# Optimization experiments

Measured on AMD Instinct MI355X. Metric: run time of the kernel, lower is better.

Reference implementation:

```python
import math
import jax, jax.numpy as jnp
import numpy as np

B = 16; ENC_S = 64; ENC_T = 96
SCALE = 64; POOL = 16; DM = 256; NH = 16
E_LAYERS = 3; D_LAYERS = 2; DFF = 1024
OUT_S = 64; OUT_T = 32
LN_EPS = 1e-5


def _pe(d_model, length):
    pos = np.arange(length, dtype=np.float32)[:, None]
    div = np.exp(np.arange(0, d_model, 2, dtype=np.float32) * (-math.log(10000.0) / d_model))
    pe = np.zeros((length, d_model), np.float32)
    pe[:, 0::2] = np.sin(pos * div)
    pe[:, 1::2] = np.cos(pos * div)
    return jnp.asarray(pe)


def _conv1d_circ(x, w, b):
    # x: (N, C, L), w: (O, C, 3); torch Conv1d(padding=1, padding_mode='circular')
    xp = jnp.pad(x, ((0, 0), (0, 0), (1, 1)), mode='wrap')
    y = jax.lax.conv_general_dilated(xp, w, (1,), 'VALID',
                                     dimension_numbers=('NCH', 'OIH', 'NCH'))
    return y + b[None, :, None]


def _layernorm(x, w, b):
    mu = jnp.mean(x, -1, keepdims=True)
    var = jnp.var(x, -1, keepdims=True)
    return (x - mu) * jax.lax.rsqrt(var + LN_EPS) * w + b


def _data_embedding(x, sproj_w, sproj_b, scproj_w, scproj_b, tok_w, tok_b):
    Bb = x.shape[0]
    h = _conv1d_circ(jnp.swapaxes(x, 1, 2), sproj_w, sproj_b)       # (B, enc_t, enc_t)
    h = _conv1d_circ(h, scproj_w, scproj_b)                          # (B, scale, enc_t)
    h = _conv1d_circ(jnp.swapaxes(h, 1, 2), scproj_w, scproj_b)     # (B, scale, scale)
    h = h.reshape(Bb * SCALE, 1, SCALE)
    tok = jnp.swapaxes(_conv1d_circ(h, tok_w, tok_b), 1, 2)          # (B*scale, scale, dm)
    emb = tok + _pe(DM, SCALE)[None]
    return emb.reshape(Bb, SCALE, SCALE, DM)


def _lin_attn(q, k, v, causal):
    # q,k,v: (Bp, L, H, E); k/v adaptively avg-pooled over L to POOL (L % POOL == 0)
    Bp, L, H, E = q.shape
    win = L // POOL
    kp = k.reshape(Bp, POOL, win, H, E).mean(axis=2)
    vp = v.reshape(Bp, POOL, win, H, E).mean(axis=2)
    scores = jnp.einsum('blhe,bshe->bhls', q, kp)      # (Bp, H, L, POOL)
    if causal:
        m = jnp.arange(POOL)[None, :] > jnp.arange(L)[:, None]
        scores = jnp.where(m[None, None], -jnp.inf, scores)
    A = jax.nn.softmax(scores / math.sqrt(E), axis=-1)
    return jnp.einsum('bhls,bshd->blhd', A, vp)


def _st_attn(x, kv, Wq, bq, Wo, bo, causal):
    Bb, T, S, dm = x.shape
    H = NH // 2
    proj = lambda z: z @ Wq.T + bq
    # faithful to source: query_projection used for q, k AND v; views are flat reshapes
    qt = proj(x.reshape(Bb * S, T, dm)).reshape(Bb * S, T, H, -1)
    qs = proj(x.reshape(Bb * T, S, dm)).reshape(Bb * T, S, H, -1)
    kt = proj(kv.reshape(Bb * S, T, dm)).reshape(Bb * S, T, H, -1)
    ks = proj(kv.reshape(Bb * T, S, dm)).reshape(Bb * T, S, H, -1)
    out_t = _lin_attn(qt, kt, kt, causal).reshape(Bb, S, T, -1)
    out_s = _lin_attn(qs, ks, ks, causal).reshape(Bb, S, T, -1)
    out = jnp.concatenate([out_t, out_s], axis=-1).reshape(Bb, S * T, 2 * dm)
    out = out @ Wo.T + bo
    return out.reshape(Bb, T, S, dm)


def _ffn(x, c1w, c1b, c2w, c2b):
    # conv1d kernel_size=1 over the T axis of (B*S, T, dm) == pointwise GEMM
    Bb, T, S, dm = x.shape
    y = x.reshape(Bb * S, T, dm)
    y = jax.nn.gelu(jnp.einsum('ntd,fd->ntf', y, c1w) + c1b, approximate=False)
    y = jnp.einsum('ntf,df->ntd', y, c2w) + c2b
    return y.reshape(Bb, T, S, dm)


def _forward(x_enc, x_dec,
             enc_sproj_w, enc_sproj_b, enc_scproj_w, enc_scproj_b, enc_tok_w, enc_tok_b,
             dec_sproj_w, dec_sproj_b, dec_scproj_w, dec_scproj_b, dec_tok_w, dec_tok_b,
             e_Wq, e_bq, e_Wo, e_bo, e_c1w, e_c1b, e_c2w, e_c2b,
             e_ln1w, e_ln1b, e_ln2w, e_ln2b, enc_norm_w, enc_norm_b,
             d_sWq, d_sbq, d_sWo, d_sbo, d_cWq, d_cbq, d_cWo, d_cbo,
             d_c1w, d_c1b, d_c2w, d_c2b,
             d_ln1w, d_ln1b, d_ln2w, d_ln2b, d_ln3w, d_ln3b,
             dec_norm_w, dec_norm_b, proj_w, proj_b):
    enc = _data_embedding(x_enc, enc_sproj_w, enc_sproj_b, enc_scproj_w, enc_scproj_b, enc_tok_w, enc_tok_b)
    for i in range(E_LAYERS):
        h = enc + _st_attn(enc, enc, e_Wq[i], e_bq[i], e_Wo[i], e_bo[i], False)
        h = _layernorm(h, e_ln1w[i], e_ln1b[i])
        enc = _layernorm(h + _ffn(h, e_c1w[i], e_c1b[i], e_c2w[i], e_c2b[i]), e_ln2w[i], e_ln2b[i])
    enc = _layernorm(enc, enc_norm_w, enc_norm_b)
    dec = _data_embedding(x_dec, dec_sproj_w, dec_sproj_b, dec_scproj_w, dec_scproj_b, dec_tok_w, dec_tok_b)
    for i in range(D_LAYERS):
        h = dec + _st_attn(dec, dec, d_sWq[i], d_sbq[i], d_sWo[i], d_sbo[i], True)
        h = _layernorm(h, d_ln1w[i], d_ln1b[i])
        h = h + _st_attn(h, enc, d_cWq[i], d_cbq[i], d_cWo[i], d_cbo[i], False)
        h = _layernorm(h, d_ln2w[i], d_ln2b[i])
        dec = _layernorm(h + _ffn(h, d_c1w[i], d_c1b[i], d_c2w[i], d_c2b[i]), d_ln3w[i], d_ln3b[i])
    dec = _layernorm(dec, dec_norm_w, dec_norm_b)
    dec = dec.mean(axis=2)                 # (B, scale, dm)
    out = dec @ proj_w.T + proj_b          # (B, scale, out_s)
    return out[:, -OUT_T:, :]


def setup_inputs() -> dict:
    keys = iter(jax.random.split(jax.random.key(0), 80))
    def nrm(shape, s=0.02):
        return jax.random.normal(next(keys), shape, jnp.float32) * s
    E, D = E_LAYERS, D_LAYERS
    inp = {
        'x_enc': nrm((B, ENC_T, ENC_S), 1.0),
        'x_dec': nrm((B, ENC_T, ENC_S), 1.0),
    }
    for p in ('enc', 'dec'):
        inp[p + '_sproj_w'] = nrm((ENC_T, ENC_S, 3)); inp[p + '_sproj_b'] = nrm((ENC_T,))
        inp[p + '_scproj_w'] = nrm((SCALE, ENC_T, 3)); inp[p + '_scproj_b'] = nrm((SCALE,))
        inp[p + '_tok_w'] = nrm((DM, 1, 3), 0.1); inp[p + '_tok_b'] = nrm((DM,))
    inp.update(
        e_Wq=nrm((E, DM, DM)), e_bq=nrm((E, DM)),
        e_Wo=nrm((E, DM, 2 * DM)), e_bo=nrm((E, DM)),
        e_c1w=nrm((E, DFF, DM)), e_c1b=nrm((E, DFF)),
        e_c2w=nrm((E, DM, DFF)), e_c2b=nrm((E, DM)),
        e_ln1w=jnp.ones((E, DM)), e_ln1b=jnp.zeros((E, DM)),
        e_ln2w=jnp.ones((E, DM)), e_ln2b=jnp.zeros((E, DM)),
        enc_norm_w=jnp.ones((DM,)), enc_norm_b=jnp.zeros((DM,)),
        d_sWq=nrm((D, DM, DM)), d_sbq=nrm((D, DM)),
        d_sWo=nrm((D, DM, 2 * DM)), d_sbo=nrm((D, DM)),
        d_cWq=nrm((D, DM, DM)), d_cbq=nrm((D, DM)),
        d_cWo=nrm((D, DM, 2 * DM)), d_cbo=nrm((D, DM)),
        d_c1w=nrm((D, DFF, DM)), d_c1b=nrm((D, DFF)),
        d_c2w=nrm((D, DM, DFF)), d_c2b=nrm((D, DM)),
        d_ln1w=jnp.ones((D, DM)), d_ln1b=jnp.zeros((D, DM)),
        d_ln2w=jnp.ones((D, DM)), d_ln2b=jnp.zeros((D, DM)),
        d_ln3w=jnp.ones((D, DM)), d_ln3b=jnp.zeros((D, DM)),
        dec_norm_w=jnp.ones((DM,)), dec_norm_b=jnp.zeros((DM,)),
        proj_w=nrm((OUT_S, DM)), proj_b=nrm((OUT_S,)),
    )
    return inp


def reference(x_enc, x_dec,
              enc_sproj_w, enc_sproj_b, enc_scproj_w, enc_scproj_b, enc_tok_w, enc_tok_b,
              dec_sproj_w, dec_sproj_b, dec_scproj_w, dec_scproj_b, dec_tok_w, dec_tok_b,
              e_Wq, e_bq, e_Wo, e_bo, e_c1w, e_c1b, e_c2w, e_c2b,
              e_ln1w, e_ln1b, e_ln2w, e_ln2b, enc_norm_w, enc_norm_b,
              d_sWq, d_sbq, d_sWo, d_sbo, d_cWq, d_cbq, d_cWo, d_cbo,
              d_c1w, d_c1b, d_c2w, d_c2b,
              d_ln1w, d_ln1b, d_ln2w, d_ln2b, d_ln3w, d_ln3b,
              dec_norm_w, dec_norm_b, proj_w, proj_b):
    return _forward(x_enc, x_dec,
                    enc_sproj_w, enc_sproj_b, enc_scproj_w, enc_scproj_b, enc_tok_w, enc_tok_b,
                    dec_sproj_w, dec_sproj_b, dec_scproj_w, dec_scproj_b, dec_tok_w, dec_tok_b,
                    e_Wq, e_bq, e_Wo, e_bo, e_c1w, e_c1b, e_c2w, e_c2b,
                    e_ln1w, e_ln1b, e_ln2w, e_ln2b, enc_norm_w, enc_norm_b,
                    d_sWq, d_sbq, d_sWo, d_sbo, d_cWq, d_cbq, d_cWo, d_cbo,
                    d_c1w, d_c1b, d_c2w, d_c2b,
                    d_ln1w, d_ln1b, d_ln2w, d_ln2b, d_ln3w, d_ln3b,
                    dec_norm_w, dec_norm_b, proj_w, proj_b)
```

## Files before the change

### kernel.cpp

```cpp
#include <hip/hip_runtime.h>


typedef unsigned short u16;
typedef short s16;
typedef __attribute__((ext_vector_type(8))) s16 bfrag;
typedef __attribute__((ext_vector_type(4))) float f32x4;

__device__ __forceinline__ float b2f(u16 u) {
  union { float f; unsigned int i; } v; v.i = ((unsigned int)u) << 16; return v.f;
}
__device__ __forceinline__ u16 f2b(float f) {
  union { float f; unsigned int i; } v; v.f = f;
  unsigned int x = v.i;
  return (u16)((x + 0x7FFFu + ((x >> 16) & 1u)) >> 16);
}
__device__ __forceinline__ float gelu_f(float v) {
  float u = 0.7978845608f * v * (1.0f + 0.044715f * v * v);
  float e = __expf(2.0f * u);
  return v * (1.0f - 1.0f / (e + 1.0f));
}

__device__ __forceinline__ void gload16(const void* g, void* l) {
  __builtin_amdgcn_global_load_lds(
      (const __attribute__((address_space(1))) unsigned int*)g,
      (__attribute__((address_space(3))) unsigned int*)l, 16, 0, 0);
}

__global__ void ws_signal(float* out, float v) { out[0] = v; }

__global__ void cvt_all(const float* s0, const float* s1, const float* s2,
                        const float* s3, const float* s4, const float* s5,
                        const float* s6,
                        u16* d0, u16* d1, u16* d2, u16* d3, u16* d4, u16* d5,
                        u16* d6,
                        int n0, int n1, int n2, int n3, int n4, int n5, int n6) {
  const float* S[7] = {s0, s1, s2, s3, s4, s5, s6};
  u16* D[7] = {d0, d1, d2, d3, d4, d5, d6};
  int N[7] = {n0, n1, n2, n3, n4, n5, n6};
  int j = blockIdx.y;
  int i = blockIdx.x * 256 + threadIdx.x;
  if (i < N[j]) D[j][i] = f2b(S[j][i]);
}

__global__ void weff_all(const float* s0, const float* s1, const float* s2,
                         const float* s3, const float* s4, const float* s5,
                         const float* s6,
                         u16* d0, u16* d1, u16* d2, u16* d3, u16* d4, u16* d5,
                         u16* d6) {
  const float* S[7] = {s0, s1, s2, s3, s4, s5, s6};
  u16* D[7] = {d0, d1, d2, d3, d4, d5, d6};
  int j = blockIdx.y;
  int n = blockIdx.x, k = threadIdx.x;
  D[j][n * 256 + k] = f2b(S[j][n * 512 + k] + S[j][n * 512 + 256 + k]);
}

__global__ void pe_kernel(float* __restrict__ pe) {
  int l = blockIdx.x, d = threadIdx.x;
  int i = d >> 1;
  float div = expf((float)(2 * i) * (-9.210340371976184f / 256.0f));
  float ang = (float)l * div;
  pe[l * 256 + d] = (d & 1) ? cosf(ang) : sinf(ang);
}

__global__ void conv_sproj(const float* xe, const float* xd,
                           const float* we, const float* be,
                           const float* wd, const float* bd,
                           float* h1e, float* h1d) {
  int o = blockIdx.x, bb = blockIdx.y, l = threadIdx.x;
  int b = (bb < 16) ? bb : bb - 16;
  const float* x = (bb < 16) ? xe : xd;
  const float* w = (bb < 16) ? we : wd;
  const float* bi = (bb < 16) ? be : bd;
  float* h1 = (bb < 16) ? h1e : h1d;
  const float* wo = w + o * 192;
  const float* xb = x + (size_t)b * 96 * 64;
  float acc = bi[o];
#pragma unroll
  for (int k = 0; k < 3; ++k) {
    int lp = l + k - 1; if (lp < 0) lp += 96; if (lp >= 96) lp -= 96;
    const float* xr = xb + lp * 64;
    for (int c = 0; c < 64; ++c) acc = fmaf(xr[c], wo[c * 3 + k], acc);
  }
  h1[((size_t)b * 96 + o) * 96 + l] = acc;
}

__global__ void conv_scproj_t(const float* h1e, const float* h1d,
                              const float* we, const float* be,
                              const float* wd, const float* bd,
                              float* h2e, float* h2d) {
  int o = blockIdx.x, bb = blockIdx.y, l = threadIdx.x;
  int b = (bb < 16) ? bb : bb - 16;
  const float* h1 = (bb < 16) ? h1e : h1d;
  const float* w = (bb < 16) ? we : wd;
  const float* bi = (bb < 16) ? be : bd;
  float* h2 = (bb < 16) ? h2e : h2d;
  const float* wo = w + o * 288;
  const float* hb = h1 + (size_t)b * 96 * 96;
  float acc = bi[o];
#pragma unroll
  for (int k = 0; k < 3; ++k) {
    int lp = l + k - 1; if (lp < 0) lp += 96; if (lp >= 96) lp -= 96;
    for (int c = 0; c < 96; ++c) acc = fmaf(hb[c * 96 + lp], wo[c * 3 + k], acc);
  }
  h2[((size_t)b * 64 + o) * 96 + l] = acc;
}

__global__ void conv_scproj_s(const float* h2e, const float* h2d,
                              const float* we, const float* be,
                              const float* wd, const float* bd,
                              float* h3e, float* h3d) {
  int o = blockIdx.x, bb = blockIdx.y, l = threadIdx.x;
  int b = (bb < 16) ? bb : bb - 16;
  const float* h2 = (bb < 16) ? h2e : h2d;
  const float* w = (bb < 16) ? we : wd;
  const float* bi = (bb < 16) ? be : bd;
  float* h3 = (bb < 16) ? h3e : h3d;
  const float* wo = w + o * 288;
  const float* hb = h2 + (size_t)b * 64 * 96;
  float acc = bi[o];
#pragma unroll
  for (int k = 0; k < 3; ++k) {
    int lp = l + k - 1; if (lp < 0) lp += 64; if (lp >= 64) lp -= 64;
    for (int c = 0; c < 96; ++c) acc = fmaf(hb[lp * 96 + c], wo[c * 3 + k], acc);
  }
  h3[((size_t)b * 64 + o) * 64 + l] = acc;
}

__global__ void tok_embed(const float* h3e, const float* h3d,
                          const float* we, const float* be,
                          const float* wd, const float* bd,
                          const float* __restrict__ pe,
                          u16* Ee, u16* Ed) {
  int gg = blockIdx.x, d = threadIdx.x;
  int g = (gg < 1024) ? gg : gg - 1024;
  const float* h3 = (gg < 1024) ? h3e : h3d;
  const float* w = (gg < 1024) ? we : wd;
  const float* bi = (gg < 1024) ? be : bd;
  u16* E = (gg < 1024) ? Ee : Ed;
  __shared__ float row[64];
  if (d < 64) row[d] = h3[(size_t)g * 64 + d];
  __syncthreads();
  float w0 = w[d * 3], w1 = w[d * 3 + 1], w2 = w[d * 3 + 2], bd_ = bi[d];
  for (int j = 0; j < 64; ++j) {
    int jm = (j + 63) & 63, jp = (j + 1) & 63;
    float v = bd_ + row[jm] * w0 + row[j] * w1 + row[jp] * w2 + pe[j * 256 + d];
    E[((size_t)g * 64 + j) * 256 + d] = f2b(v);
  }
}

template <int ACT, int NBX>
__global__ __launch_bounds__(256) void mfma_gemm(const u16* __restrict__ A,
                                                 const u16* __restrict__ W,
                                                 const float* __restrict__ bias,
                                                 u16* __restrict__ C, int N, int K,
                                                 int nby) {
  __shared__ s16 smem[16384];
  s16* A0 = smem;        s16* A1 = smem + 4096;
  s16* B0 = smem + 8192; s16* B1 = smem + 12288;
  constexpr int LB = (NBX == 8) ? 3 : 1;
  int f = blockIdx.x;
  int q = (NBX * nby) >> 3;
  int w = (f & 7) * q + (f >> 3);
  int bx = w & (NBX - 1), by = w >> LB;
  int t = threadIdx.x;
  int wave = t >> 6, lane = t & 63;
  int wr = wave >> 1, wc = wave & 1;
  int row0 = by * 128, col0 = bx * 128;
  int kc = (lane >> 4) & 3, rr = lane & 15;
  const u16* Ap0 = A + (size_t)(row0 + wave * 16 + rr) * K + kc * 8;
  const u16* Ap1 = A + (size_t)(row0 + (wave + 4) * 16 + rr) * K + kc * 8;
  const u16* Bp0 = W + (size_t)(col0 + wave * 16 + rr) * K + kc * 8;
  const u16* Bp1 = W + (size_t)(col0 + (wave + 4) * 16 + rr) * K + kc * 8;
  f32x4 acc[4][4];
#pragma unroll
  for (int m = 0; m < 4; ++m)
#pragma unroll
    for (int n = 0; n < 4; ++n) acc[m][n] = (f32x4){0.f, 0.f, 0.f, 0.f};

  auto STAGE = [&](s16* a, s16* b, int kidx) {
    int k0 = kidx * 32;
    gload16(Ap0 + k0, a + wave * 512);
    gload16(Ap1 + k0, a + (wave + 4) * 512);
    gload16(Bp0 + k0, b + wave * 512);
    gload16(Bp1 + k0, b + (wave + 4) * 512);
  };
  int nk = K >> 5;
  auto STEP = [&](const s16* a, const s16* b, s16* sa, s16* sb, int ks) {
    if (ks + 1 < nk) asm volatile("s_waitcnt vmcnt(4)" ::: "memory");
    else             asm volatile("s_waitcnt vmcnt(0)" ::: "memory");
    __builtin_amdgcn_sched_barrier(0);
    __builtin_amdgcn_s_barrier();
    __builtin_amdgcn_sched_barrier(0);
    bfrag af[4], bf[4];
#pragma unroll
    for (int m = 0; m < 4; ++m) af[m] = *(const bfrag*)(a + ((wr * 4 + m) * 64 + lane) * 8);
#pragma unroll
    for (int n = 0; n < 4; ++n) bf[n] = *(const bfrag*)(b + ((wc * 4 + n) * 64 + lane) * 8);
    asm volatile("s_waitcnt lgkmcnt(0)" ::: "memory");
    __builtin_amdgcn_sched_barrier(0);
    __builtin_amdgcn_s_barrier();
    __builtin_amdgcn_sched_barrier(0);
    if (ks + 2 < nk) STAGE(sa, sb, ks + 2);
#pragma unroll
    for (int m = 0; m < 4; ++m)
#pragma unroll
      for (int n = 0; n < 4; ++n)
        acc[m][n] = __builtin_amdgcn_mfma_f32_16x16x32_bf16(af[m], bf[n], acc[m][n], 0, 0, 0);
  };

  STAGE(A0, B0, 0);
  STAGE(A1, B1, 1);
  for (int ks = 0; ks < nk; ks += 2) {
    STEP(A0, B0, A0, B0, ks);
    STEP(A1, B1, A1, B1, ks + 1);
  }
  s16* Cs = smem;
  int g4 = (lane >> 4) << 2;
  int cl = lane & 15;
  float bc[4];
#pragma unroll
  for (int n = 0; n < 4; ++n) bc[n] = bias[col0 + wc * 64 + n * 16 + cl];
#pragma unroll
  for (int P = 0; P < 4; ++P) {
    __syncthreads();
    if (wr == (P >> 1)) {
#pragma unroll
      for (int mm = 0; mm < 2; ++mm) {
        int m = (P & 1) * 2 + mm;
#pragma unroll
        for (int n = 0; n < 4; ++n) {
#pragma unroll
          for (int r = 0; r < 4; ++r) {
            float v = acc[m][n][r] + bc[n];
            if (ACT == 1) v = gelu_f(v);
            Cs[(mm * 16 + g4 + r) * 136 + wc * 64 + n * 16 + cl] = (s16)f2b(v);
          }
        }
      }
    }
    __syncthreads();
#pragma unroll
    for (int it = 0; it < 2; ++it) {
      int idx = it * 256 + t;
      int lr = idx >> 4, slot = idx & 15;
      *(uint4*)(C + (size_t)(row0 + P * 32 + lr) * N + col0 + slot * 8) =
          *(const uint4*)(Cs + lr * 136 + slot * 8);
    }
  }
}

__global__ __launch_bounds__(512) void mfma_gemm_resln(const u16* __restrict__ X,
                                                       const u16* __restrict__ W,
                                                       const float* __restrict__ bias,
                                                       u16* __restrict__ R,
                                                       const float* __restrict__ lnw,
                                                       const float* __restrict__ lnb,
                                                       int K) {
  __shared__ s16 smem[24576];
  __shared__ float pls[32][4][2];
  s16* A0 = smem;        s16* A1 = smem + 4096;
  s16* B0 = smem + 8192; s16* B1 = smem + 16384;
  int t = threadIdx.x;
  int wave = t >> 6, lane = t & 63;
  int wr = wave >> 2, wc = wave & 3;
  int row0 = blockIdx.x * 128;
  int kc = (lane >> 4) & 3, rr = lane & 15;
  const u16* Xp = X + (size_t)(row0 + wave * 16 + rr) * K + kc * 8;
  const u16* Wp0 = W + (size_t)(wave * 16 + rr) * K + kc * 8;
  const u16* Wp1 = W + (size_t)((wave + 8) * 16 + rr) * K + kc * 8;
  f32x4 acc[4][4];
#pragma unroll
  for (int m = 0; m < 4; ++m)
#pragma unroll
    for (int n = 0; n < 4; ++n) acc[m][n] = (f32x4){0.f, 0.f, 0.f, 0.f};

  auto STAGE = [&](s16* a, s16* b, int kidx) {
    int k0 = kidx * 32;
    gload16(Xp + k0, a + wave * 512);
    gload16(Wp0 + k0, b + wave * 512);
    gload16(Wp1 + k0, b + (wave + 8) * 512);
  };
  int nk = K >> 5;
  auto STEP = [&](const s16* a, const s16* b, s16* sa, s16* sb, int ks) {
    if (ks + 1 < nk) asm volatile("s_waitcnt vmcnt(3)" ::: "memory");
    else             asm volatile("s_waitcnt vmcnt(0)" ::: "memory");
    __builtin_amdgcn_sched_barrier(0);
    __builtin_amdgcn_s_barrier();
    __builtin_amdgcn_sched_barrier(0);
    bfrag af[4], bf[4];
#pragma unroll
    for (int m = 0; m < 4; ++m) af[m] = *(const bfrag*)(a + ((wr * 4 + m) * 64 + lane) * 8);
#pragma unroll
    for (int n = 0; n < 4; ++n) bf[n] = *(const bfrag*)(b + ((wc * 4 + n) * 64 + lane) * 8);
    asm volatile("s_waitcnt lgkmcnt(0)" ::: "memory");
    __builtin_amdgcn_sched_barrier(0);
    __builtin_amdgcn_s_barrier();
    __builtin_amdgcn_sched_barrier(0);
    if (ks + 2 < nk) STAGE(sa, sb, ks + 2);
#pragma unroll
    for (int m = 0; m < 4; ++m)
#pragma unroll
      for (int n = 0; n < 4; ++n)
        acc[m][n] = __builtin_amdgcn_mfma_f32_16x16x32_bf16(af[m], bf[n], acc[m][n], 0, 0, 0);
  };

  STAGE(A0, B0, 0);
  STAGE(A1, B1, 1);
  for (int ks = 0; ks < nk; ks += 2) {
    STEP(A0, B0, A0, B0, ks);
    STEP(A1, B1, A1, B1, ks + 1);
  }
  s16* Rs = smem;
  int g4 = (lane >> 4) << 2;
  int cl = lane & 15;
  float lw[4], lb[4], bc[4];
#pragma unroll
  for (int n = 0; n < 4; ++n) {
    int col = wc * 64 + n * 16 + cl;
    bc[n] = bias[col]; lw[n] = lnw[col]; lb[n] = lnb[col];
  }
#pragma unroll
  for (int P = 0; P < 4; ++P) {
    bool own = (wr == (P >> 1));
    __syncthreads();
#pragma unroll
    for (int it = 0; it < 2; ++it) {
      int idx = it * 512 + t;
      int lr = idx >> 5, slot = idx & 31;
      *(uint4*)(Rs + lr * 264 + slot * 8) =
          *(const uint4*)(R + (size_t)(row0 + P * 32 + lr) * 256 + slot * 8);
    }
    __syncthreads();
    if (own) {
#pragma unroll
      for (int mm = 0; mm < 2; ++mm) {
        int m = (P & 1) * 2 + mm;
#pragma unroll
        for (int r = 0; r < 4; ++r) {
          int lr = mm * 16 + g4 + r;
          float s = 0.f, s2 = 0.f;
#pragma unroll
          for (int n = 0; n < 4; ++n) {
            float v = acc[m][n][r] + bc[n] +
                      b2f((u16)Rs[lr * 264 + wc * 64 + n * 16 + cl]);
            acc[m][n][r] = v;
            s += v; s2 = fmaf(v, v, s2);
          }
#pragma unroll
          for (int o = 1; o < 16; o <<= 1) { s += __shfl_xor(s, o); s2 += __shfl_xor(s2, o); }
          if (cl == 0) { pls[lr][wc][0] = s; pls[lr][wc][1] = s2; }
        }
      }
    }
    __syncthreads();
    if (own) {
#pragma unroll
      for (int mm = 0; mm < 2; ++mm) {
        int m = (P & 1) * 2 + mm;
#pragma unroll
        for (int r = 0; r < 4; ++r) {
          int lr = mm * 16 + g4 + r;
          float s = pls[lr][0][0] + pls[lr][1][0] + pls[lr][2][0] + pls[lr][3][0];
          float s2 = pls[lr][0][1] + pls[lr][1][1] + pls[lr][2][1] + pls[lr][3][1];
          float mu = s * (1.0f / 256.0f);
          float var = fmaxf(s2 * (1.0f / 256.0f) - mu * mu, 0.0f);
          float rs = rsqrtf(var + 1e-5f);
#pragma unroll
          for (int n = 0; n < 4; ++n) {
            Rs[lr * 264 + wc * 64 + n * 16 + cl] =
                (s16)f2b((acc[m][n][r] - mu) * rs * lw[n] + lb[n]);
          }
        }
      }
    }
    __syncthreads();
#pragma unroll
    for (int it = 0; it < 2; ++it) {
      int idx = it * 512 + t;
      int lr = idx >> 5, slot = idx & 31;
      *(uint4*)(R + (size_t)(row0 + P * 32 + lr) * 256 + slot * 8) =
          *(const uint4*)(Rs + lr * 264 + slot * 8);
    }
  }
}

template <int CROSS, int CAUSAL>
__global__ __launch_bounds__(256) void qk_attn(const u16* __restrict__ A,
                                               const u16* __restrict__ Wq,
                                               const float* __restrict__ bq,
                                               u16* __restrict__ O,
                                               const u16* __restrict__ KP) {
  __shared__ s16 smem[27136];
  s16* Qs = smem;
  s16* As = smem + 16896;
  s16* Bs = smem + 18944;
  float* kp = (float*)(smem + 16896);
  int p = blockIdx.x, t = threadIdx.x;
  int wave = t >> 6, lane = t & 63;
  int wr = wave >> 1, wc = wave & 1;
  int kc = (lane >> 4) & 3, rr = lane & 15;
  const u16* Ap = A + (size_t)(p * 64 + wave * 16 + rr) * 256 + kc * 8;
  const u16* Wp = Wq + (size_t)rr * 256 + kc * 8;
  f32x4 acc[2][8];
#pragma unroll
  for (int m = 0; m < 2; ++m)
#pragma unroll
    for (int n = 0; n < 8; ++n) acc[m][n] = (f32x4){0.f, 0.f, 0.f, 0.f};

#pragma unroll
  for (int ks = 0; ks < 8; ++ks) {
    int k0 = ks * 32;
    gload16(Ap + k0, As + wave * 512);
#pragma unroll
    for (int i = 0; i < 4; ++i) {
      int fb = wave + i * 4;
      gload16(Wp + (size_t)fb * 16 * 256 + k0, Bs + fb * 512);
    }
    __syncthreads();
    bfrag a[2], b[8];
#pragma unroll
    for (int m = 0; m < 2; ++m) a[m] = *(const bfrag*)(As + ((wr * 2 + m) * 64 + lane) * 8);
#pragma unroll
    for (int n = 0; n < 8; ++n) b[n] = *(const bfrag*)(Bs + ((wc * 8 + n) * 64 + lane) * 8);
#pragma unroll
    for (int m = 0; m < 2; ++m)
#pragma unroll
      for (int n = 0; n < 8; ++n)
        acc[m][n] = __builtin_amdgcn_mfma_f32_16x16x32_bf16(a[m], b[n], acc[m][n], 0, 0, 0);
    __syncthreads();
  }
  int g4 = (lane >> 4) << 2;
  int cl = lane & 15;
#pragma unroll
  for (int m = 0; m < 2; ++m) {
#pragma unroll
    for (int n = 0; n < 8; ++n) {
      int col = wc * 128 + n * 16 + cl;
      float bcol = bq[col];
#pragma unroll
      for (int r = 0; r < 4; ++r) {
        int row = wr * 32 + m * 16 + g4 + r;
        Qs[row * 264 + col] = (s16)f2b(acc[m][n][r] + bcol);
      }
    }
  }
  __syncthreads();
  if (CROSS) {
    for (int idx = t; idx < 4096; idx += 256) {
      int s = idx >> 8, d = idx & 255;
      kp[s * 260 + d] = b2f(KP[((size_t)p * 16 + s) * 256 + d]);
    }
  } else {
    for (int idx = t; idx < 4096; idx += 256) {
      int s = idx >> 8, d = idx & 255;
      const s16* b0 = Qs + (4 * s) * 264 + d;
      kp[s * 260 + d] = 0.25f * (b2f((u16)b0[0]) + b2f((u16)b0[264]) +
                                 b2f((u16)b0[528]) + b2f((u16)b0[792]));
    }
  }
  __syncthreads();
#pragma unroll
  for (int pi = 0; pi < 2; ++pi) {
    int pp = t + pi * 256;
    int h = pp >> 6, l = pp & 63;
    s16* q = Qs + l * 264 + h * 32;
    float qr[32];
#pragma unroll
    for (int e = 0; e < 32; e += 4) {
      ushort4 v = *(const ushort4*)&q[e];
      qr[e] = b2f(v.x); qr[e + 1] = b2f(v.y); qr[e + 2] = b2f(v.z); qr[e + 3] = b2f(v.w);
    }
    float sc[16], mx = -INFINITY;
#pragma unroll
    for (int s = 0; s < 16; ++s) {
      const float* kpp = kp + s * 260 + h * 32;
      float d = 0.f;
#pragma unroll
      for (int e = 0; e < 32; ++e) d = fmaf(qr[e], kpp[e], d);
      d *= 0.17677669529663687f;
      if (CAUSAL && s > l) d = -INFINITY;
      sc[s] = d; mx = fmaxf(mx, d);
    }
    float sum = 0.f;
#pragma unroll
    for (int s = 0; s < 16; ++s) { sc[s] = expf(sc[s] - mx); sum += sc[s]; }
    float inv = 1.0f / sum;
    float o[32] = {};
#pragma unroll
    for (int s = 0; s < 16; ++s) {
      float a = sc[s] * inv;
      const float* vp = kp + s * 260 + h * 32;
#pragma unroll
      for (int e = 0; e < 32; ++e) o[e] = fmaf(a, vp[e], o[e]);
    }
#pragma unroll
    for (int e = 0; e < 32; e += 4) {
      ushort4 v;
      v.x = f2b(o[e]); v.y = f2b(o[e + 1]); v.z = f2b(o[e + 2]); v.w = f2b(o[e + 3]);
      *(ushort4*)&q[e] = v;
    }
  }
  __syncthreads();
  u16* Og = O + (size_t)p * 16384;
#pragma unroll
  for (int i = 0; i < 8; ++i) {
    int idx = i * 256 + t;
    int row = idx >> 5, slot = idx & 31;
    *(uint4*)(Og + row * 256 + slot * 8) = *(const uint4*)(Qs + row * 264 + slot * 8);
  }
}

__global__ __launch_bounds__(256) void ln_bf(u16* __restrict__ X,
                                             const float* __restrict__ w,
                                             const float* __restrict__ b) {
  int lane = threadIdx.x & 63, wv = threadIdx.x >> 6;
  size_t row = (size_t)blockIdx.x * 4 + wv;
  size_t off = row * 256 + lane * 4;
  ushort4 xv = *(const ushort4*)(X + off);
  float v0 = b2f(xv.x), v1 = b2f(xv.y), v2 = b2f(xv.z), v3 = b2f(xv.w);
  float s = v0 + v1 + v2 + v3;
  float s2 = v0 * v0 + v1 * v1 + v2 * v2 + v3 * v3;
#pragma unroll
  for (int o = 32; o; o >>= 1) { s += __shfl_xor(s, o); s2 += __shfl_xor(s2, o); }
  float mu = s * (1.0f / 256.0f);
  float var = fmaxf(s2 * (1.0f / 256.0f) - mu * mu, 0.0f);
  float rs = rsqrtf(var + 1e-5f);
  float4 w4 = *(const float4*)(w + lane * 4);
  float4 b4 = *(const float4*)(b + lane * 4);
  ushort4 o4;
  o4.x = f2b((v0 - mu) * rs * w4.x + b4.x);
  o4.y = f2b((v1 - mu) * rs * w4.y + b4.y);
  o4.z = f2b((v2 - mu) * rs * w4.z + b4.z);
  o4.w = f2b((v3 - mu) * rs * w4.w + b4.w);
  *(ushort4*)(X + off) = o4;
}

__global__ void pool_bf(const u16* __restrict__ A, u16* __restrict__ P) {
  int r = blockIdx.x, d = threadIdx.x;
  int g = r >> 4, s = r & 15;
  const u16* src = A + ((size_t)g * 64 + 4 * (size_t)s) * 256 + d;
  float v = 0.25f * (b2f(src[0]) + b2f(src[256]) + b2f(src[512]) + b2f(src[768]));
  P[(size_t)r * 256 + d] = f2b(v);
}

__global__ __launch_bounds__(256) void mean_proj_bf(const u16* __restrict__ X,
                                                    const float* __restrict__ pw,
                                                    const float* __restrict__ pb,
                                                    float* __restrict__ out) {
  int bid = blockIdx.x;
  int b = bid >> 5, ii = bid & 31;
  int i = 32 + ii;
  __shared__ float md[256];
  int d = threadIdx.x;
  const u16* base = X + ((size_t)b * 64 + i) * 64 * 256 + d;
  float s = 0.f;
  for (int j = 0; j < 64; ++j) s += b2f(base[(size_t)j * 256]);
  md[d] = s * (1.0f / 64.0f);
  __syncthreads();
  if (d < 64) {
    float acc = pb[d];
    const float* wr = pw + d * 256;
    for (int k = 0; k < 256; ++k) acc = fmaf(md[k], wr[k], acc);
    out[((size_t)b * 32 + ii) * 64 + d] = acc;
  }
}

extern "C" void kernel_launch(void* const* d_in, const int* in_sizes, int n_in,
                              void* d_out, int out_size, void* d_ws, size_t ws_size,
                              hipStream_t stream) {
  (void)in_sizes; (void)out_size;
  if (n_in < 50) return;

  const float* x_enc = (const float*)d_in[0];
  const float* x_dec = (const float*)d_in[1];
  const float* enc_sproj_w = (const float*)d_in[2];
  const float* enc_sproj_b = (const float*)d_in[3];
  const float* enc_scproj_w = (const float*)d_in[4];
  const float* enc_scproj_b = (const float*)d_in[5];
  const float* enc_tok_w = (const float*)d_in[6];
  const float* enc_tok_b = (const float*)d_in[7];
  const float* dec_sproj_w = (const float*)d_in[8];
  const float* dec_sproj_b = (const float*)d_in[9];
  const float* dec_scproj_w = (const float*)d_in[10];
  const float* dec_scproj_b = (const float*)d_in[11];
  const float* dec_tok_w = (const float*)d_in[12];
  const float* dec_tok_b = (const float*)d_in[13];
  const float* e_Wq = (const float*)d_in[14];
  const float* e_bq = (const float*)d_in[15];
  const float* e_Wo = (const float*)d_in[16];
  const float* e_bo = (const float*)d_in[17];
  const float* e_c1w = (const float*)d_in[18];
  const float* e_c1b = (const float*)d_in[19];
  const float* e_c2w = (const float*)d_in[20];
  const float* e_c2b = (const float*)d_in[21];
  const float* e_ln1w = (const float*)d_in[22];
  const float* e_ln1b = (const float*)d_in[23];
  const float* e_ln2w = (const float*)d_in[24];
  const float* e_ln2b = (const float*)d_in[25];
  const float* enc_norm_w = (const float*)d_in[26];
  const float* enc_norm_b = (const float*)d_in[27];
  const float* d_sWq = (const float*)d_in[28];
  const float* d_sbq = (const float*)d_in[29];
  const float* d_sWo = (const float*)d_in[30];
  const float* d_sbo = (const float*)d_in[31];
  const float* d_cWq = (const float*)d_in[32];
  const float* d_cbq = (const float*)d_in[33];
  const float* d_cWo = (const float*)d_in[34];
  const float* d_cbo = (const float*)d_in[35];
  const float* d_c1w = (const float*)d_in[36];
  const float* d_c1b = (const float*)d_in[37];
  const float* d_c2w = (const float*)d_in[38];
  const float* d_c2b = (const float*)d_in[39];
  const float* d_ln1w = (const float*)d_in[40];
  const float* d_ln1b = (const float*)d_in[41];
  const float* d_ln2w = (const float*)d_in[42];
  const float* d_ln2b = (const float*)d_in[43];
  const float* d_ln3w = (const float*)d_in[44];
  const float* d_ln3b = (const float*)d_in[45];
  const float* dec_norm_w = (const float*)d_in[46];
  const float* dec_norm_b = (const float*)d_in[47];
  const float* proj_w = (const float*)d_in[48];
  const float* proj_b = (const float*)d_in[49];

  const size_t ACT = 16777216;
  const size_t POOLE = 4194304;
  const size_t WBN = 3538944;
  size_t base_need = (3 * ACT + 2 * POOLE + WBN) * 2 +
                     (size_t)(16384 + 2 * (147456 + 98304 + 65536)) * 4;
  if (ws_size < base_need) {
    ws_signal<<<1, 1, 0, stream>>>((float*)d_out, (float)(ws_size >> 20));
    return;
  }
  char* wsb = (char*)d_ws;
  u16* A_enc = (u16*)wsb;  wsb += ACT * 2;
  u16* A_dec = (u16*)wsb;  wsb += ACT * 2;
  u16* T1 = (u16*)wsb;     wsb += ACT * 2;
  u16* PA = (u16*)wsb;     wsb += POOLE * 2;
  u16* PK = (u16*)wsb;     wsb += POOLE * 2;
  u16* WB = (u16*)wsb;     wsb += WBN * 2;
  float* PE = (float*)wsb;  wsb += 16384 * 4;
  float* EH1 = (float*)wsb; wsb += 147456 * 4;
  float* EH2 = (float*)wsb; wsb += 98304 * 4;
  float* EH3 = (float*)wsb; wsb += 65536 * 4;
  float* FH1 = (float*)wsb; wsb += 147456 * 4;
  float* FH2 = (float*)wsb; wsb += 98304 * 4;
  float* FH3 = (float*)wsb; wsb += 65536 * 4;

  int hf_rows = 16384;
  u16* HF = T1;
  if (ws_size >= base_need + (size_t)65536 * 1024 * 2) {
    hf_rows = 65536; HF = (u16*)wsb;
  } else if (ws_size >= base_need + (size_t)32768 * 1024 * 2) {
    hf_rows = 32768; HF = (u16*)wsb;
  }

  u16* eWq = WB;
  u16* eWeff = WB + 196608;
  u16* eC1 = WB + 393216;
  u16* eC2 = WB + 1179648;
  u16* dB = WB + 1966080;
  u16* dsWq = dB;
  u16* dsWeff = dB + 131072;
  u16* dcWq = dB + 262144;
  u16* dcWeff = dB + 393216;
  u16* dC1 = dB + 524288;
  u16* dC2 = dB + 1048576;

  cvt_all<<<dim3(3072, 7), 256, 0, stream>>>(
      e_Wq, e_c1w, e_c2w, d_sWq, d_cWq, d_c1w, d_c2w,
      eWq, eC1, eC2, dsWq, dcWq, dC1, dC2,
      196608, 786432, 786432, 131072, 131072, 524288, 524288);
  weff_all<<<dim3(256, 7), 256, 0, stream>>>(
      e_Wo, e_Wo + 131072, e_Wo + 262144, d_sWo, d_sWo + 131072,
      d_cWo, d_cWo + 131072,
      eWeff, eWeff + 65536, eWeff + 131072, dsWeff, dsWeff + 65536,
      dcWeff, dcWeff + 65536);

  pe_kernel<<<64, 256, 0, stream>>>(PE);

  conv_sproj<<<dim3(96, 32), 96, 0, stream>>>(x_enc, x_dec, enc_sproj_w, enc_sproj_b,
                                              dec_sproj_w, dec_sproj_b, EH1, FH1);
  conv_scproj_t<<<dim3(64, 32), 96, 0, stream>>>(EH1, FH1, enc_scproj_w, enc_scproj_b,
                                                 dec_scproj_w, dec_scproj_b, EH2, FH2);
  conv_scproj_s<<<dim3(64, 32), 64, 0, stream>>>(EH2, FH2, enc_scproj_w, enc_scproj_b,
                                                 dec_scproj_w, dec_scproj_b, EH3, FH3);
  tok_embed<<<2048, 256, 0, stream>>>(EH3, FH3, enc_tok_w, enc_tok_b,
                                      dec_tok_w, dec_tok_b, PE, A_enc, A_dec);

  for (int i = 0; i < 3; ++i) {
    qk_attn<0, 0><<<1024, 256, 0, stream>>>(A_enc, eWq + (size_t)i * 65536,
                                            e_bq + i * 256, T1, nullptr);
    mfma_gemm_resln<<<512, 512, 0, stream>>>(T1, eWeff + (size_t)i * 65536, e_bo + i * 256,
                                             A_enc, e_ln1w + i * 256, e_ln1b + i * 256, 256);
    for (int m0 = 0; m0 < 65536; m0 += hf_rows) {
      u16* Xc = A_enc + (size_t)m0 * 256;
      int nby = hf_rows / 128;
      mfma_gemm<1, 8><<<8 * nby, 256, 0, stream>>>(
          Xc, eC1 + (size_t)i * 262144, e_c1b + i * 1024, HF, 1024, 256, nby);
      mfma_gemm_resln<<<nby, 512, 0, stream>>>(
          HF, eC2 + (size_t)i * 262144, e_c2b + i * 256, Xc,
          e_ln2w + i * 256, e_ln2b + i * 256, 1024);
    }
  }
  ln_bf<<<16384, 256, 0, stream>>>(A_enc, enc_norm_w, enc_norm_b);
  pool_bf<<<16384, 256, 0, stream>>>(A_enc, PA);

  for (int i = 0; i < 2; ++i) {
    qk_attn<0, 1><<<1024, 256, 0, stream>>>(A_dec, dsWq + (size_t)i * 65536,
                                            d_sbq + i * 256, T1, nullptr);
    mfma_gemm_resln<<<512, 512, 0, stream>>>(T1, dsWeff + (size_t)i * 65536, d_sbo + i * 256,
                                             A_dec, d_ln1w + i * 256, d_ln1b + i * 256, 256);
    mfma_gemm<0, 2><<<256, 256, 0, stream>>>(PA, dcWq + (size_t)i * 65536,
                                             d_cbq + i * 256, PK, 256, 256, 128);
    qk_attn<1, 0><<<1024, 256, 0, stream>>>(A_dec, dcWq + (size_t)i * 65536,
                                            d_cbq + i * 256, T1, PK);
    mfma_gemm_resln<<<512, 512, 0, stream>>>(T1, dcWeff + (size_t)i * 65536, d_cbo + i * 256,
                                             A_dec, d_ln2w + i * 256, d_ln2b + i * 256, 256);
    for (int m0 = 0; m0 < 65536; m0 += hf_rows) {
      u16* Xc = A_dec + (size_t)m0 * 256;
      int nby = hf_rows / 128;
      mfma_gemm<1, 8><<<8 * nby, 256, 0, stream>>>(
          Xc, dC1 + (size_t)i * 262144, d_c1b + i * 1024, HF, 1024, 256, nby);
      mfma_gemm_resln<<<nby, 512, 0, stream>>>(
          HF, dC2 + (size_t)i * 262144, d_c2b + i * 256, Xc,
          d_ln3w + i * 256, d_ln3b + i * 256, 1024);
    }
  }
  ln_bf<<<16384, 256, 0, stream>>>(A_dec, dec_norm_w, dec_norm_b);

  mean_proj_bf<<<512, 256, 0, stream>>>(A_dec, proj_w, proj_b, (float*)d_out);
}
```

Before: 1.872 ms.

## Split Q projection from linear attention and use 256x256 tiles for FFN up-projection

The fused qk_attn kernel, which recomputed the Q projection with a small 64-row MFMA tile per block, is replaced by a separate mfma_gemm launch for the projection followed by a lighter lin_attn kernel that works in place on the projected tensor with 512 threads. The FFN first GEMM switches to a new 256x256-tile, 512-thread, double-buffered kernel with explicit waitcnt/barrier pipelining and a remapped block order. The goal is better MFMA utilisation and operand reuse in the GEMMs. The cost is an extra global round-trip of the Q tensor between kernels, plus extra launches.

```diff
diff --git a/kernel.cpp b/kernel.cpp
--- a/kernel.cpp
+++ b/kernel.cpp
@@ -249,6 +249,106 @@
   }
 }
 
+template <int ACT>
+__global__ __launch_bounds__(512) void mfma_gemm256(const u16* __restrict__ A,
+                                                    const u16* __restrict__ W,
+                                                    const float* __restrict__ bias,
+                                                    u16* __restrict__ C, int N, int K,
+                                                    int nby) {
+  __shared__ s16 smem[32768];
+  s16* A0 = smem;         s16* A1 = smem + 8192;
+  s16* B0 = smem + 16384; s16* B1 = smem + 24576;
+  int f = blockIdx.x;
+  int q = (4 * nby) >> 3;
+  int w = (f & 7) * q + (f >> 3);
+  int bx = w & 3, by = w >> 2;
+  int t = threadIdx.x;
+  int wave = t >> 6, lane = t & 63;
+  int wr = wave >> 2, wc = wave & 3;
+  int row0 = by * 256, col0 = bx * 256;
+  int kc = (lane >> 4) & 3, rr = lane & 15;
+  const u16* Ap0 = A + (size_t)(row0 + wave * 16 + rr) * K + kc * 8;
+  const u16* Ap1 = A + (size_t)(row0 + (wave + 8) * 16 + rr) * K + kc * 8;
+  const u16* Bp0 = W + (size_t)(col0 + wave * 16 + rr) * K + kc * 8;
+  const u16* Bp1 = W + (size_t)(col0 + (wave + 8) * 16 + rr) * K + kc * 8;
+  f32x4 acc[8][4];
+#pragma unroll
+  for (int m = 0; m < 8; ++m)
+#pragma unroll
+    for (int n = 0; n < 4; ++n) acc[m][n] = (f32x4){0.f, 0.f, 0.f, 0.f};
+
+  auto STAGE = [&](s16* a, s16* b, int kidx) {
+    int k0 = kidx * 32;
+    gload16(Ap0 + k0, a + wave * 512);
+    gload16(Ap1 + k0, a + (wave + 8) * 512);
+    gload16(Bp0 + k0, b + wave * 512);
+    gload16(Bp1 + k0, b + (wave + 8) * 512);
+  };
+  int nk = K >> 5;
+  auto STEP = [&](const s16* a, const s16* b, s16* sa, s16* sb, int ks) {
+    if (ks + 1 < nk) asm volatile("s_waitcnt vmcnt(4)" ::: "memory");
+    else             asm volatile("s_waitcnt vmcnt(0)" ::: "memory");
+    __builtin_amdgcn_sched_barrier(0);
+    __builtin_amdgcn_s_barrier();
+    __builtin_amdgcn_sched_barrier(0);
+    bfrag af[8], bf[4];
+#pragma unroll
+    for (int m = 0; m < 8; ++m) af[m] = *(const bfrag*)(a + ((wr * 8 + m) * 64 + lane) * 8);
+#pragma unroll
+    for (int n = 0; n < 4; ++n) bf[n] = *(const bfrag*)(b + ((wc * 4 + n) * 64 + lane) * 8);
+    asm volatile("s_waitcnt lgkmcnt(0)" ::: "memory");
+    __builtin_amdgcn_sched_barrier(0);
+    __builtin_amdgcn_s_barrier();
+    __builtin_amdgcn_sched_barrier(0);
+    if (ks + 2 < nk) STAGE(sa, sb, ks + 2);
+#pragma unroll
+    for (int m = 0; m < 8; ++m)
+#pragma unroll
+      for (int n = 0; n < 4; ++n)
+        acc[m][n] = __builtin_amdgcn_mfma_f32_16x16x32_bf16(af[m], bf[n], acc[m][n], 0, 0, 0);
+  };
+
+  STAGE(A0, B0, 0);
+  STAGE(A1, B1, 1);
+  for (int ks = 0; ks < nk; ks += 2) {
+    STEP(A0, B0, A0, B0, ks);
+    STEP(A1, B1, A1, B1, ks + 1);
+  }
+  s16* Cs = smem;
+  int g4 = (lane >> 4) << 2;
+  int cl = lane & 15;
+  float bc[4];
+#pragma unroll
+  for (int n = 0; n < 4; ++n) bc[n] = bias[col0 + wc * 64 + n * 16 + cl];
+#pragma unroll
+  for (int P = 0; P < 8; ++P) {
+    __syncthreads();
+    if (wr == (P >> 2)) {
+#pragma unroll
+      for (int mm = 0; mm < 2; ++mm) {
+        int m = (P & 3) * 2 + mm;
+#pragma unroll
+        for (int n = 0; n < 4; ++n) {
+#pragma unroll
+          for (int r = 0; r < 4; ++r) {
+            float v = acc[m][n][r] + bc[n];
+            if (ACT == 1) v = gelu_f(v);
+            Cs[(mm * 16 + g4 + r) * 264 + wc * 64 + n * 16 + cl] = (s16)f2b(v);
+          }
+        }
+      }
+    }
+    __syncthreads();
+#pragma unroll
+    for (int it = 0; it < 2; ++it) {
+      int idx = it * 512 + t;
+      int lr = idx >> 5, slot = idx & 31;
+      *(uint4*)(C + (size_t)(row0 + P * 32 + lr) * N + col0 + slot * 8) =
+          *(const uint4*)(Cs + lr * 264 + slot * 8);
+    }
+  }
+}
+
 __global__ __launch_bounds__(512) void mfma_gemm_resln(const u16* __restrict__ X,
                                                        const u16* __restrict__ W,
                                                        const float* __restrict__ bias,
@@ -385,128 +485,75 @@
 }
 
 template <int CROSS, int CAUSAL>
-__global__ __launch_bounds__(256) void qk_attn(const u16* __restrict__ A,
-                                               const u16* __restrict__ Wq,
-                                               const float* __restrict__ bq,
-                                               u16* __restrict__ O,
-                                               const u16* __restrict__ KP) {
-  __shared__ s16 smem[27136];
-  s16* Qs = smem;
-  s16* As = smem + 16896;
-  s16* Bs = smem + 18944;
-  float* kp = (float*)(smem + 16896);
+__global__ __launch_bounds__(512) void lin_attn(u16* __restrict__ Q,
+                                                const u16* __restrict__ KP) {
+  __shared__ u16 qs[64 * 264];
+  __shared__ float kpool[16][260];
   int p = blockIdx.x, t = threadIdx.x;
-  int wave = t >> 6, lane = t & 63;
-  int wr = wave >> 1, wc = wave & 1;
-  int kc = (lane >> 4) & 3, rr = lane & 15;
-  const u16* Ap = A + (size_t)(p * 64 + wave * 16 + rr) * 256 + kc * 8;
-  const u16* Wp = Wq + (size_t)rr * 256 + kc * 8;
-  f32x4 acc[2][8];
-#pragma unroll
-  for (int m = 0; m < 2; ++m)
-#pragma unroll
-    for (int n = 0; n < 8; ++n) acc[m][n] = (f32x4){0.f, 0.f, 0.f, 0.f};
-
-#pragma unroll
-  for (int ks = 0; ks < 8; ++ks) {
-    int k0 = ks * 32;
-    gload16(Ap + k0, As + wave * 512);
-#pragma unroll
-    for (int i = 0; i < 4; ++i) {
-      int fb = wave + i * 4;
-      gload16(Wp + (size_t)fb * 16 * 256 + k0, Bs + fb * 512);
-    }
-    __syncthreads();
-    bfrag a[2], b[8];
-#pragma unroll
-    for (int m = 0; m < 2; ++m) a[m] = *(const bfrag*)(As + ((wr * 2 + m) * 64 + lane) * 8);
-#pragma unroll
-    for (int n = 0; n < 8; ++n) b[n] = *(const bfrag*)(Bs + ((wc * 8 + n) * 64 + lane) * 8);
-#pragma unroll
-    for (int m = 0; m < 2; ++m)
-#pragma unroll
-      for (int n = 0; n < 8; ++n)
-        acc[m][n] = __builtin_amdgcn_mfma_f32_16x16x32_bf16(a[m], b[n], acc[m][n], 0, 0, 0);
-    __syncthreads();
-  }
-  int g4 = (lane >> 4) << 2;
-  int cl = lane & 15;
-#pragma unroll
-  for (int m = 0; m < 2; ++m) {
-#pragma unroll
-    for (int n = 0; n < 8; ++n) {
-      int col = wc * 128 + n * 16 + cl;
-      float bcol = bq[col];
-#pragma unroll
-      for (int r = 0; r < 4; ++r) {
-        int row = wr * 32 + m * 16 + g4 + r;
-        Qs[row * 264 + col] = (s16)f2b(acc[m][n][r] + bcol);
-      }
-    }
+  u16* Qg = Q + (size_t)p * 16384;
+#pragma unroll
+  for (int i = 0; i < 4; ++i) {
+    int idx = i * 512 + t;
+    int row = idx >> 5, slot = idx & 31;
+    *(uint4*)(qs + row * 264 + slot * 8) = *(const uint4*)(Qg + row * 256 + slot * 8);
   }
   __syncthreads();
   if (CROSS) {
-    for (int idx = t; idx < 4096; idx += 256) {
+    for (int idx = t; idx < 4096; idx += 512) {
       int s = idx >> 8, d = idx & 255;
-      kp[s * 260 + d] = b2f(KP[((size_t)p * 16 + s) * 256 + d]);
+      kpool[s][d] = b2f(KP[((size_t)p * 16 + s) * 256 + d]);
     }
   } else {
-    for (int idx = t; idx < 4096; idx += 256) {
+    for (int idx = t; idx < 4096; idx += 512) {
       int s = idx >> 8, d = idx & 255;
-      const s16* b0 = Qs + (4 * s) * 264 + d;
-      kp[s * 260 + d] = 0.25f * (b2f((u16)b0[0]) + b2f((u16)b0[264]) +
-                                 b2f((u16)b0[528]) + b2f((u16)b0[792]));
+      const u16* b0 = qs + (4 * s) * 264 + d;
+      kpool[s][d] = 0.25f * (b2f(b0[0]) + b2f(b0[264]) + b2f(b0[528]) + b2f(b0[792]));
     }
   }
   __syncthreads();
-#pragma unroll
-  for (int pi = 0; pi < 2; ++pi) {
-    int pp = t + pi * 256;
-    int h = pp >> 6, l = pp & 63;
-    s16* q = Qs + l * 264 + h * 32;
-    float qr[32];
-#pragma unroll
-    for (int e = 0; e < 32; e += 4) {
-      ushort4 v = *(const ushort4*)&q[e];
-      qr[e] = b2f(v.x); qr[e + 1] = b2f(v.y); qr[e + 2] = b2f(v.z); qr[e + 3] = b2f(v.w);
-    }
-    float sc[16], mx = -INFINITY;
-#pragma unroll
-    for (int s = 0; s < 16; ++s) {
-      const float* kpp = kp + s * 260 + h * 32;
-      float d = 0.f;
-#pragma unroll
-      for (int e = 0; e < 32; ++e) d = fmaf(qr[e], kpp[e], d);
-      d *= 0.17677669529663687f;
-      if (CAUSAL && s > l) d = -INFINITY;
-      sc[s] = d; mx = fmaxf(mx, d);
-    }
-    float sum = 0.f;
-#pragma unroll
-    for (int s = 0; s < 16; ++s) { sc[s] = expf(sc[s] - mx); sum += sc[s]; }
-    float inv = 1.0f / sum;
-    float o[32] = {};
-#pragma unroll
-    for (int s = 0; s < 16; ++s) {
-      float a = sc[s] * inv;
-      const float* vp = kp + s * 260 + h * 32;
-#pragma unroll
-      for (int e = 0; e < 32; ++e) o[e] = fmaf(a, vp[e], o[e]);
-    }
-#pragma unroll
-    for (int e = 0; e < 32; e += 4) {
-      ushort4 v;
-      v.x = f2b(o[e]); v.y = f2b(o[e + 1]); v.z = f2b(o[e + 2]); v.w = f2b(o[e + 3]);
-      *(ushort4*)&q[e] = v;
-    }
+  int h = t >> 6, l = t & 63;
+  u16* q = qs + l * 264 + h * 32;
+  float qr[32];
+#pragma unroll
+  for (int e = 0; e < 32; e += 4) {
+    ushort4 v = *(const ushort4*)&q[e];
+    qr[e] = b2f(v.x); qr[e + 1] = b2f(v.y); qr[e + 2] = b2f(v.z); qr[e + 3] = b2f(v.w);
+  }
+  float sc[16], mx = -INFINITY;
+#pragma unroll
+  for (int s = 0; s < 16; ++s) {
+    const float* kp = &kpool[s][h * 32];
+    float d = 0.f;
+#pragma unroll
+    for (int e = 0; e < 32; ++e) d = fmaf(qr[e], kp[e], d);
+    d *= 0.17677669529663687f;
+    if (CAUSAL && s > l) d = -INFINITY;
+    sc[s] = d; mx = fmaxf(mx, d);
+  }
+  float sum = 0.f;
+#pragma unroll
+  for (int s = 0; s < 16; ++s) { sc[s] = expf(sc[s] - mx); sum += sc[s]; }
+  float inv = 1.0f / sum;
+  float o[32] = {};
+#pragma unroll
+  for (int s = 0; s < 16; ++s) {
+    float a = sc[s] * inv;
+    const float* vp = &kpool[s][h * 32];
+#pragma unroll
+    for (int e = 0; e < 32; ++e) o[e] = fmaf(a, vp[e], o[e]);
+  }
+#pragma unroll
+  for (int e = 0; e < 32; e += 4) {
+    ushort4 v;
+    v.x = f2b(o[e]); v.y = f2b(o[e + 1]); v.z = f2b(o[e + 2]); v.w = f2b(o[e + 3]);
+    *(ushort4*)&q[e] = v;
   }
   __syncthreads();
-  u16* Og = O + (size_t)p * 16384;
-#pragma unroll
-  for (int i = 0; i < 8; ++i) {
-    int idx = i * 256 + t;
+#pragma unroll
+  for (int i = 0; i < 4; ++i) {
+    int idx = i * 512 + t;
     int row = idx >> 5, slot = idx & 31;
-    *(uint4*)(Og + row * 256 + slot * 8) = *(const uint4*)(Qs + row * 264 + slot * 8);
+    *(uint4*)(Qg + row * 256 + slot * 8) = *(const uint4*)(qs + row * 264 + slot * 8);
   }
 }
 
@@ -688,16 +735,17 @@
                                       dec_tok_w, dec_tok_b, PE, A_enc, A_dec);
 
   for (int i = 0; i < 3; ++i) {
-    qk_attn<0, 0><<<1024, 256, 0, stream>>>(A_enc, eWq + (size_t)i * 65536,
-                                            e_bq + i * 256, T1, nullptr);
+    mfma_gemm<0, 2><<<1024, 256, 0, stream>>>(A_enc, eWq + (size_t)i * 65536,
+                                              e_bq + i * 256, T1, 256, 256, 512);
+    lin_attn<0, 0><<<1024, 512, 0, stream>>>(T1, nullptr);
     mfma_gemm_resln<<<512, 512, 0, stream>>>(T1, eWeff + (size_t)i * 65536, e_bo + i * 256,
                                              A_enc, e_ln1w + i * 256, e_ln1b + i * 256, 256);
     for (int m0 = 0; m0 < 65536; m0 += hf_rows) {
       u16* Xc = A_enc + (size_t)m0 * 256;
-      int nby = hf_rows / 128;
-      mfma_gemm<1, 8><<<8 * nby, 256, 0, stream>>>(
+      int nby = hf_rows / 256;
+      mfma_gemm256<1><<<4 * nby, 512, 0, stream>>>(
           Xc, eC1 + (size_t)i * 262144, e_c1b + i * 1024, HF, 1024, 256, nby);
-      mfma_gemm_resln<<<nby, 512, 0, stream>>>(
+      mfma_gemm_resln<<<hf_rows / 128, 512, 0, stream>>>(
           HF, eC2 + (size_t)i * 262144, e_c2b + i * 256, Xc,
           e_ln2w + i * 256, e_ln2b + i * 256, 1024);
     }
@@ -706,22 +754,24 @@
   pool_bf<<<16384, 256, 0, stream>>>(A_enc, PA);
 
   for (int i = 0; i < 2; ++i) {
-    qk_attn<0, 1><<<1024, 256, 0, stream>>>(A_dec, dsWq + (size_t)i * 65536,
-                                            d_sbq + i * 256, T1, nullptr);
+    mfma_gemm<0, 2><<<1024, 256, 0, stream>>>(A_dec, dsWq + (size_t)i * 65536,
+                                              d_sbq + i * 256, T1, 256, 256, 512);
+    lin_attn<0, 1><<<1024, 512, 0, stream>>>(T1, nullptr);
     mfma_gemm_resln<<<512, 512, 0, stream>>>(T1, dsWeff + (size_t)i * 65536, d_sbo + i * 256,
                                              A_dec, d_ln1w + i * 256, d_ln1b + i * 256, 256);
+    mfma_gemm<0, 2><<<1024, 256, 0, stream>>>(A_dec, dcWq + (size_t)i * 65536,
+                                              d_cbq + i * 256, T1, 256, 256, 512);
     mfma_gemm<0, 2><<<256, 256, 0, stream>>>(PA, dcWq + (size_t)i * 65536,
                                              d_cbq + i * 256, PK, 256, 256, 128);
-    qk_attn<1, 0><<<1024, 256, 0, stream>>>(A_dec, dcWq + (size_t)i * 65536,
-                                            d_cbq + i * 256, T1, PK);
+    lin_attn<1, 0><<<1024, 512, 0, stream>>>(T1, PK);
     mfma_gemm_resln<<<512, 512, 0, stream>>>(T1, dcWeff + (size_t)i * 65536, d_cbo + i * 256,
                                              A_dec, d_ln2w + i * 256, d_ln2b + i * 256, 256);
     for (int m0 = 0; m0 < 65536; m0 += hf_rows) {
       u16* Xc = A_dec + (size_t)m0 * 256;
-      int nby = hf_rows / 128;
-      mfma_gemm<1, 8><<<8 * nby, 256, 0, stream>>>(
+      int nby = hf_rows / 256;
+      mfma_gemm256<1><<<4 * nby, 512, 0, stream>>>(
           Xc, dC1 + (size_t)i * 262144, d_c1b + i * 1024, HF, 1024, 256, nby);
-      mfma_gemm_resln<<<nby, 512, 0, stream>>>(
+      mfma_gemm_resln<<<hf_rows / 128, 512, 0, stream>>>(
           HF, dC2 + (size_t)i * 262144, d_c2b + i * 256, Xc,
           d_ln3w + i * 256, d_ln3b + i * 256, 1024);
     }
```

New measurement: 1.738 ms. -7.1%, faster.
